# Kernel tuning notes

Measured on AMD Instinct MI355X. Metric: run time of the kernel, lower is better.

Reference implementation:

```python
import jax, jax.numpy as jnp
import numpy as np

# SpikingJelly LIFNode defaults
TAU = 2.0        # membrane time constant
V_TH = 1.0       # threshold
ALPHA = 2.0      # ATan surrogate alpha (forward is pure Heaviside)
T_STEPS = 4
OBS_DIM, CTX_DIM, ACT_DIM, HID = 128, 64, 32, 1024
OUTPUT_MAX = 1.0


def spike_fn(x):
    # forward-only Heaviside (surrogate only matters for backward)
    return (x >= 0.0).astype(x.dtype)


def lif_layer(x_seq):
    """Multi-step LIF: x_seq [T,B,H] -> spikes [T,B,H].
    decay_input=True: v = v + (x - (v - v_reset)) / tau; hard reset to v_reset=0."""
    def step(v, x):
        v = v + (x - v) / TAU
        s = spike_fn(v - V_TH)
        v = v * (1.0 - s)  # hard reset to 0
        return v, s
    v0 = jnp.zeros_like(x_seq[0])
    _, s_seq = jax.lax.scan(step, v0, x_seq)
    return s_seq


def setup_inputs() -> dict:
    key = jax.random.key(0)
    ks = jax.random.split(key, 12)
    B = 16384
    obs = jax.random.normal(ks[0], (B, OBS_DIM), dtype=jnp.float32)
    context = jax.random.normal(ks[1], (B, CTX_DIM), dtype=jnp.float32)
    # noise ~ N(0, 0.001) clamped later in reference
    noise = jax.random.normal(ks[2], (ACT_DIM,), dtype=jnp.float32) * 0.001
    in_dim = OBS_DIM + CTX_DIM
    def xavier(k, fan_in, fan_out, gain=0.1):
        bound = gain * np.sqrt(6.0 / (fan_in + fan_out))
        return jax.random.uniform(k, (fan_out, fan_in), jnp.float32, -bound, bound)
    W1 = xavier(ks[3], in_dim, HID); b1 = jnp.zeros((HID,), jnp.float32)
    W2 = xavier(ks[4], HID, HID);   b2 = jnp.zeros((HID,), jnp.float32)
    W3 = xavier(ks[5], HID, HID);   b3 = jnp.zeros((HID,), jnp.float32)
    Wm = xavier(ks[6], HID, ACT_DIM); bm = jnp.zeros((ACT_DIM,), jnp.float32)
    return {"obs": obs, "context": context, "noise": noise,
            "W1": W1, "b1": b1, "W2": W2, "b2": b2,
            "W3": W3, "b3": b3, "Wm": Wm, "bm": bm}


def reference(obs, context, noise, W1, b1, W2, b2, W3, b3, Wm, bm):
    x = jnp.concatenate([obs, context], axis=-1)           # [B, in_dim]
    x_seq = jnp.broadcast_to(x, (T_STEPS,) + x.shape)      # [T, B, in_dim]
    h = lif_layer(jnp.einsum('tbi,oi->tbo', x_seq, W1) + b1)
    h = lif_layer(jnp.einsum('tbh,oh->tbo', h, W2) + b2)
    h = lif_layer(jnp.einsum('tbh,oh->tbo', h, W3) + b3)
    feat = h.mean(axis=0)                                   # [B, HID]
    action_mean = OUTPUT_MAX * jnp.tanh(feat @ Wm.T + bm)   # [B, ACT_DIM]
    action = action_mean + jnp.clip(noise, -0.1, 0.1)
    return (action_mean, action)
```

## Files before the change

kernel.cpp:

```cpp
#include <hip/hip_runtime.h>
#include <stdint.h>
#include <math.h>

#define NB 16384


__global__ __launch_bounds__(256) void kA(
    const float* __restrict__ W1, const float* __restrict__ b1,
    const float* __restrict__ b2, const float* __restrict__ b3,
    const float* __restrict__ W3, const float* __restrict__ Wm,
    const float* __restrict__ bm, const float* __restrict__ noise,
    float* __restrict__ ws_f, unsigned int* __restrict__ ws_u)
{
  const int bid = blockIdx.x, tid = threadIdx.x;
  if (bid < 256) {
    const int wv = tid >> 6, lane = tid & 63;
    const int r = bid * 4 + wv;
    float ss = 0.f;
    if (lane < 48) {
      float4 v = *(const float4*)(W1 + (size_t)r * 192 + lane * 4);
      ss = v.x * v.x + v.y * v.y + v.z * v.z + v.w * v.w;
    }
    #pragma unroll
    for (int off = 32; off; off >>= 1) ss += __shfl_down(ss, off);
    if (lane == 0) atomicMax(&ws_u[1], __float_as_uint(ss));
    return;
  }
  if (bid == 256) {
    float m = 0.f;
    #pragma unroll
    for (int g = 0; g < 4; ++g) m = fmaxf(m, fabsf(b1[tid + 256 * g]));
    atomicMax(&ws_u[2], __float_as_uint(m));
    return;
  }
  __shared__ unsigned int m2[4][32];
  __shared__ unsigned int F2[4];
  __shared__ float feat[1024];
  __shared__ int fnz;
  if (tid < 128) ((unsigned int*)m2)[tid] = 0u;
  if (tid == 0) fnz = 0;
  __syncthreads();
  #pragma unroll
  for (int g = 0; g < 4; ++g) {
    const int o = tid + 256 * g;
    const float c = b2[o];
    float v = 0.f;
    #pragma unroll
    for (int t = 0; t < 4; ++t) {
      v = v + (c - v) * 0.5f;
      if (v >= 1.0f) { atomicOr(&m2[t][o >> 5], 1u << (o & 31)); v = 0.f; }
    }
  }
  __syncthreads();
  if (tid < 4) {
    unsigned int f = 0;
    #pragma unroll
    for (int w = 0; w < 32; ++w) f |= m2[tid][w];
    F2[tid] = f;
  }
  __syncthreads();
  #pragma unroll
  for (int g = 0; g < 4; ++g) {
    const int o = tid + 256 * g;
    const float cb = b3[o];
    float v = 0.f, fs = 0.f;
    #pragma unroll
    for (int t = 0; t < 4; ++t) {
      float c = cb;
      if (F2[t]) {
        for (int wl = 0; wl < 32; ++wl) {
          unsigned int mm = m2[t][wl];
          while (mm) {
            const int k = wl * 32 + __builtin_ctz(mm);
            c += W3[(size_t)o * 1024 + k];
            mm &= (mm - 1);
          }
        }
      }
      v = v + (c - v) * 0.5f;
      if (v >= 1.0f) { fs += 1.0f; v = 0.f; }
    }
    feat[o] = fs * 0.25f;
    if (fs > 0.f) fnz = 1;
  }
  __syncthreads();
  if (tid < 32) {
    float acc = 0.f;
    if (fnz) {
      const float* wr = Wm + (size_t)tid * 1024;
      for (int k = 0; k < 1024; ++k) acc += feat[k] * wr[k];
    }
    const float z = acc + bm[tid];
    const float am = tanhf(z);
    const float nz = fminf(fmaxf(noise[tid], -0.1f), 0.1f);
    ws_f[64 + tid] = am;
    ws_f[96 + tid] = am + nz;
  }
}

__global__ __launch_bounds__(256) void kMain(
    const float* __restrict__ obs, const float* __restrict__ ctx,
    const float* __restrict__ ws_f, const unsigned int* __restrict__ ws_u,
    int* __restrict__ ws_i, float* __restrict__ out)
{
  const int tid = threadIdx.x;
  if (blockIdx.x < 4096) {
    const int wv = tid >> 6, lane = tid & 63;
    const int r = blockIdx.x * 4 + wv;
    float ss = 0.f;
    if (lane < 32) {
      float4 v = ((const float4*)(obs + (size_t)r * 128))[lane];
      ss = v.x * v.x + v.y * v.y + v.z * v.z + v.w * v.w;
    } else if (lane < 48) {
      float4 v = ((const float4*)(ctx + (size_t)r * 64))[lane - 32];
      ss = v.x * v.x + v.y * v.y + v.z * v.z + v.w * v.w;
    }
    #pragma unroll
    for (int off = 32; off; off >>= 1) ss += __shfl_down(ss, off);
    if (lane == 0) {
      const float wm2 = __uint_as_float(ws_u[1]);
      const float bmx = __uint_as_float(ws_u[2]);
      const float bound = sqrtf(ss) * sqrtf(wm2) * 1.0001f + bmx + 1e-5f;
      if (bound >= 1.0666f) {
        const int idx = atomicAdd(&ws_i[0], 1);
        ws_i[256 + idx] = r;
      }
    }
    return;
  }
  const int t = (blockIdx.x - 4096) * 256 + tid;
  const int row = t >> 3, q = t & 7;
  float4 av = ((const float4*)(ws_f + 64))[q];
  float4 cv = ((const float4*)(ws_f + 96))[q];
  ((float4*)out)[(size_t)row * 8 + q] = av;
  ((float4*)(out + (size_t)NB * 32))[(size_t)row * 8 + q] = cv;
}

__global__ __launch_bounds__(256) void kFB(
    const float* __restrict__ obs, const float* __restrict__ ctx,
    const float* __restrict__ noise,
    const float* __restrict__ W1, const float* __restrict__ b1,
    const float* __restrict__ W2, const float* __restrict__ b2,
    const float* __restrict__ W3, const float* __restrict__ b3,
    const float* __restrict__ Wm, const float* __restrict__ bm,
    const int* __restrict__ ws_i, float* __restrict__ out)
{
  __shared__ float x[192];
  __shared__ unsigned int mm[2][4][32];
  __shared__ unsigned int F[2][4];
  __shared__ float feat[1024];
  const int tid = threadIdx.x;
  const int cnt = ws_i[0];
  for (int i = blockIdx.x; i < cnt; i += 64) {
    const int b = ws_i[256 + i];
    if (tid < 192)
      x[tid] = (tid < 128) ? obs[(size_t)b * 128 + tid]
                           : ctx[(size_t)b * 64 + (tid - 128)];
    ((unsigned int*)mm)[tid] = 0u;
    __syncthreads();
    #pragma unroll
    for (int g = 0; g < 4; ++g) {
      const int o = tid + 256 * g;
      float c = b1[o];
      const float* w = W1 + (size_t)o * 192;
      for (int k = 0; k < 192; ++k) c += x[k] * w[k];
      float v = 0.f;
      #pragma unroll
      for (int t = 0; t < 4; ++t) {
        v = v + (c - v) * 0.5f;
        if (v >= 1.0f) { atomicOr(&mm[0][t][o >> 5], 1u << (o & 31)); v = 0.f; }
      }
    }
    __syncthreads();
    if (tid < 8) {
      unsigned int f = 0;
      #pragma unroll
      for (int w = 0; w < 32; ++w) f |= mm[tid >> 2][tid & 3][w];
      F[tid >> 2][tid & 3] = f;
    }
    __syncthreads();
    #pragma unroll
    for (int g = 0; g < 4; ++g) {
      const int o = tid + 256 * g;
      const float cb = b2[o];
      float v = 0.f;
      #pragma unroll
      for (int t = 0; t < 4; ++t) {
        float c = cb;
        if (F[0][t]) {
          for (int wl = 0; wl < 32; ++wl) {
            unsigned int m = mm[0][t][wl];
            while (m) {
              const int k = wl * 32 + __builtin_ctz(m);
              c += W2[(size_t)o * 1024 + k];
              m &= (m - 1);
            }
          }
        }
        v = v + (c - v) * 0.5f;
        if (v >= 1.0f) { atomicOr(&mm[1][t][o >> 5], 1u << (o & 31)); v = 0.f; }
      }
    }
    __syncthreads();
    if (tid < 4) {
      unsigned int f = 0;
      #pragma unroll
      for (int w = 0; w < 32; ++w) f |= mm[1][tid][w];
      F[1][tid] = f;
    }
    __syncthreads();
    #pragma unroll
    for (int g = 0; g < 4; ++g) {
      const int o = tid + 256 * g;
      const float cb = b3[o];
      float v = 0.f, fs = 0.f;
      #pragma unroll
      for (int t = 0; t < 4; ++t) {
        float c = cb;
        if (F[1][t]) {
          for (int wl = 0; wl < 32; ++wl) {
            unsigned int m = mm[1][t][wl];
            while (m) {
              const int k = wl * 32 + __builtin_ctz(m);
              c += W3[(size_t)o * 1024 + k];
              m &= (m - 1);
            }
          }
        }
        v = v + (c - v) * 0.5f;
        if (v >= 1.0f) { fs += 1.0f; v = 0.f; }
      }
      feat[o] = fs * 0.25f;
    }
    __syncthreads();
    if (tid < 32) {
      const float* wr = Wm + (size_t)tid * 1024;
      float acc = 0.f;
      for (int k = 0; k < 1024; ++k) acc += feat[k] * wr[k];
      const float z = acc + bm[tid];
      const float am = tanhf(z);
      const float nz = fminf(fmaxf(noise[tid], -0.1f), 0.1f);
      out[(size_t)b * 32 + tid] = am;
      out[(size_t)NB * 32 + (size_t)b * 32 + tid] = am + nz;
    }
    __syncthreads();
  }
}

extern "C" void kernel_launch(void* const* d_in, const int* in_sizes, int n_in,
                              void* d_out, int out_size, void* d_ws, size_t ws_size,
                              hipStream_t stream) {
  const float* obs   = (const float*)d_in[0];
  const float* ctx   = (const float*)d_in[1];
  const float* noise = (const float*)d_in[2];
  const float* W1    = (const float*)d_in[3];
  const float* b1    = (const float*)d_in[4];
  const float* W2    = (const float*)d_in[5];
  const float* b2    = (const float*)d_in[6];
  const float* W3    = (const float*)d_in[7];
  const float* b3    = (const float*)d_in[8];
  const float* Wm    = (const float*)d_in[9];
  const float* bm    = (const float*)d_in[10];
  float* out = (float*)d_out;

  float*        ws_f = (float*)d_ws;
  unsigned int* ws_u = (unsigned int*)d_ws;
  int*          ws_i = (int*)d_ws;

  hipMemsetAsync(d_ws, 0, 64, stream);
  kA<<<258, 256, 0, stream>>>(W1, b1, b2, b3, W3, Wm, bm, noise, ws_f, ws_u);
  kMain<<<4608, 256, 0, stream>>>(obs, ctx, ws_f, ws_u, ws_i, out);
  kFB<<<64, 256, 0, stream>>>(obs, ctx, noise, W1, b1, W2, b2, W3, b3, Wm, bm,
                              ws_i, out);
}
```

Before: 103.7 us.

## Fuse bound check, broadcast store and fallback into one per-row kernel

Merges the row-norm bound kernel and the fallback kernel into a single kernel, kRow. In it each wavefront checks its own row and either writes the precomputed constant output or runs the full spiking MLP inline, using ballot-based sparse accumulation. The global atomicMax reductions are replaced by per-block partial maxima that each wave reduces again itself, which removes the workspace memset and the global atomic row-index queue. This cuts one launch and the memset. In exchange, any fallback row runs on a single wavefront with uncoalesced weight reads, which would be slow if many rows need the full path.

```diff
diff --git a/kernel.cpp b/kernel.cpp
--- a/kernel.cpp
+++ b/kernel.cpp
@@ -10,10 +10,11 @@
     const float* __restrict__ b2, const float* __restrict__ b3,
     const float* __restrict__ W3, const float* __restrict__ Wm,
     const float* __restrict__ bm, const float* __restrict__ noise,
-    float* __restrict__ ws_f, unsigned int* __restrict__ ws_u)
+    float* __restrict__ ws_f)
 {
   const int bid = blockIdx.x, tid = threadIdx.x;
   if (bid < 256) {
+    __shared__ float pm[4];
     const int wv = tid >> 6, lane = tid & 63;
     const int r = bid * 4 + wv;
     float ss = 0.f;
@@ -23,14 +24,24 @@
     }
     #pragma unroll
     for (int off = 32; off; off >>= 1) ss += __shfl_down(ss, off);
-    if (lane == 0) atomicMax(&ws_u[1], __float_as_uint(ss));
+    if (lane == 0) pm[wv] = ss;
+    __syncthreads();
+    if (tid == 0)
+      ws_f[bid] = fmaxf(fmaxf(pm[0], pm[1]), fmaxf(pm[2], pm[3]));
     return;
   }
   if (bid == 256) {
+    __shared__ float pm[4];
+    const int wv = tid >> 6, lane = tid & 63;
     float m = 0.f;
     #pragma unroll
     for (int g = 0; g < 4; ++g) m = fmaxf(m, fabsf(b1[tid + 256 * g]));
-    atomicMax(&ws_u[2], __float_as_uint(m));
+    #pragma unroll
+    for (int off = 32; off; off >>= 1) m = fmaxf(m, __shfl_down(m, off));
+    if (lane == 0) pm[wv] = m;
+    __syncthreads();
+    if (tid == 0)
+      ws_f[256] = fmaxf(fmaxf(pm[0], pm[1]), fmaxf(pm[2], pm[3]));
     return;
   }
   __shared__ unsigned int m2[4][32];
@@ -93,157 +104,117 @@
     const float z = acc + bm[tid];
     const float am = tanhf(z);
     const float nz = fminf(fmaxf(noise[tid], -0.1f), 0.1f);
-    ws_f[64 + tid] = am;
-    ws_f[96 + tid] = am + nz;
+    ws_f[512 + tid] = am;
+    ws_f[544 + tid] = am + nz;
   }
 }
 
-__global__ __launch_bounds__(256) void kMain(
-    const float* __restrict__ obs, const float* __restrict__ ctx,
-    const float* __restrict__ ws_f, const unsigned int* __restrict__ ws_u,
-    int* __restrict__ ws_i, float* __restrict__ out)
-{
-  const int tid = threadIdx.x;
-  if (blockIdx.x < 4096) {
-    const int wv = tid >> 6, lane = tid & 63;
-    const int r = blockIdx.x * 4 + wv;
-    float ss = 0.f;
-    if (lane < 32) {
-      float4 v = ((const float4*)(obs + (size_t)r * 128))[lane];
-      ss = v.x * v.x + v.y * v.y + v.z * v.z + v.w * v.w;
-    } else if (lane < 48) {
-      float4 v = ((const float4*)(ctx + (size_t)r * 64))[lane - 32];
-      ss = v.x * v.x + v.y * v.y + v.z * v.z + v.w * v.w;
-    }
-    #pragma unroll
-    for (int off = 32; off; off >>= 1) ss += __shfl_down(ss, off);
-    if (lane == 0) {
-      const float wm2 = __uint_as_float(ws_u[1]);
-      const float bmx = __uint_as_float(ws_u[2]);
-      const float bound = sqrtf(ss) * sqrtf(wm2) * 1.0001f + bmx + 1e-5f;
-      if (bound >= 1.0666f) {
-        const int idx = atomicAdd(&ws_i[0], 1);
-        ws_i[256 + idx] = r;
-      }
-    }
-    return;
-  }
-  const int t = (blockIdx.x - 4096) * 256 + tid;
-  const int row = t >> 3, q = t & 7;
-  float4 av = ((const float4*)(ws_f + 64))[q];
-  float4 cv = ((const float4*)(ws_f + 96))[q];
-  ((float4*)out)[(size_t)row * 8 + q] = av;
-  ((float4*)(out + (size_t)NB * 32))[(size_t)row * 8 + q] = cv;
-}
-
-__global__ __launch_bounds__(256) void kFB(
+__global__ __launch_bounds__(256) void kRow(
     const float* __restrict__ obs, const float* __restrict__ ctx,
     const float* __restrict__ noise,
     const float* __restrict__ W1, const float* __restrict__ b1,
     const float* __restrict__ W2, const float* __restrict__ b2,
     const float* __restrict__ W3, const float* __restrict__ b3,
     const float* __restrict__ Wm, const float* __restrict__ bm,
-    const int* __restrict__ ws_i, float* __restrict__ out)
+    const float* __restrict__ ws_f, float* __restrict__ out)
 {
-  __shared__ float x[192];
-  __shared__ unsigned int mm[2][4][32];
-  __shared__ unsigned int F[2][4];
-  __shared__ float feat[1024];
   const int tid = threadIdx.x;
-  const int cnt = ws_i[0];
-  for (int i = blockIdx.x; i < cnt; i += 64) {
-    const int b = ws_i[256 + i];
-    if (tid < 192)
-      x[tid] = (tid < 128) ? obs[(size_t)b * 128 + tid]
-                           : ctx[(size_t)b * 64 + (tid - 128)];
-    ((unsigned int*)mm)[tid] = 0u;
-    __syncthreads();
-    #pragma unroll
-    for (int g = 0; g < 4; ++g) {
-      const int o = tid + 256 * g;
-      float c = b1[o];
-      const float* w = W1 + (size_t)o * 192;
-      for (int k = 0; k < 192; ++k) c += x[k] * w[k];
-      float v = 0.f;
-      #pragma unroll
-      for (int t = 0; t < 4; ++t) {
-        v = v + (c - v) * 0.5f;
-        if (v >= 1.0f) { atomicOr(&mm[0][t][o >> 5], 1u << (o & 31)); v = 0.f; }
+  const int wv = tid >> 6, lane = tid & 63;
+  const int r = blockIdx.x * 4 + wv;
+
+  float ss = 0.f;
+  if (lane < 32) {
+    float4 v = ((const float4*)(obs + (size_t)r * 128))[lane];
+    ss = v.x * v.x + v.y * v.y + v.z * v.z + v.w * v.w;
+  } else if (lane < 48) {
+    float4 v = ((const float4*)(ctx + (size_t)r * 64))[lane - 32];
+    ss = v.x * v.x + v.y * v.y + v.z * v.z + v.w * v.w;
+  }
+  #pragma unroll
+  for (int off = 32; off; off >>= 1) ss += __shfl_xor(ss, off);
+
+  float wm2 = fmaxf(fmaxf(ws_f[lane], ws_f[lane + 64]),
+                    fmaxf(ws_f[lane + 128], ws_f[lane + 192]));
+  #pragma unroll
+  for (int off = 32; off; off >>= 1) wm2 = fmaxf(wm2, __shfl_xor(wm2, off));
+  const float bmx = ws_f[256];
+
+  const float bound = sqrtf(ss) * sqrtf(wm2) * 1.0001f + bmx + 1e-5f;
+
+  if (bound < 1.0666f) {
+    if (lane < 8)
+      ((float4*)out)[(size_t)r * 8 + lane] = ((const float4*)(ws_f + 512))[lane];
+    else if (lane < 16)
+      ((float4*)(out + (size_t)NB * 32))[(size_t)r * 8 + (lane - 8)] =
+          ((const float4*)(ws_f + 544))[lane - 8];
+    return;
+  }
+
+  unsigned long long s1b = 0ull;
+  for (int g = 0; g < 16; ++g) {
+    const int o = lane + 64 * g;
+    float c = b1[o];
+    const float* w = W1 + (size_t)o * 192;
+    for (int k = 0; k < 128; ++k) c += obs[(size_t)r * 128 + k] * w[k];
+    for (int k = 0; k < 64; ++k)  c += ctx[(size_t)r * 64 + k] * w[128 + k];
+    float v = 0.f;
+    #pragma unroll
+    for (int t = 0; t < 4; ++t) {
+      v = v + (c - v) * 0.5f;
+      if (v >= 1.0f) { s1b |= 1ull << (g * 4 + t); v = 0.f; }
+    }
+  }
+  unsigned long long s2b = 0ull;
+  for (int g = 0; g < 16; ++g) {
+    const int o = lane + 64 * g;
+    float v = 0.f;
+    for (int t = 0; t < 4; ++t) {
+      float c = b2[o];
+      for (int i = 0; i < 16; ++i) {
+        unsigned long long w = __ballot((s1b >> (i * 4 + t)) & 1ull);
+        while (w) {
+          const int k = 64 * i + __builtin_ctzll(w);
+          c += W2[(size_t)o * 1024 + k];
+          w &= (w - 1);
+        }
       }
-    }
-    __syncthreads();
-    if (tid < 8) {
-      unsigned int f = 0;
-      #pragma unroll
-      for (int w = 0; w < 32; ++w) f |= mm[tid >> 2][tid & 3][w];
-      F[tid >> 2][tid & 3] = f;
-    }
-    __syncthreads();
-    #pragma unroll
-    for (int g = 0; g < 4; ++g) {
-      const int o = tid + 256 * g;
-      const float cb = b2[o];
-      float v = 0.f;
-      #pragma unroll
-      for (int t = 0; t < 4; ++t) {
-        float c = cb;
-        if (F[0][t]) {
-          for (int wl = 0; wl < 32; ++wl) {
-            unsigned int m = mm[0][t][wl];
-            while (m) {
-              const int k = wl * 32 + __builtin_ctz(m);
-              c += W2[(size_t)o * 1024 + k];
-              m &= (m - 1);
-            }
-          }
+      v = v + (c - v) * 0.5f;
+      if (v >= 1.0f) { s2b |= 1ull << (g * 4 + t); v = 0.f; }
+    }
+  }
+  float feat[16];
+  for (int g = 0; g < 16; ++g) {
+    const int o = lane + 64 * g;
+    float v = 0.f, fs = 0.f;
+    for (int t = 0; t < 4; ++t) {
+      float c = b3[o];
+      for (int i = 0; i < 16; ++i) {
+        unsigned long long w = __ballot((s2b >> (i * 4 + t)) & 1ull);
+        while (w) {
+          const int k = 64 * i + __builtin_ctzll(w);
+          c += W3[(size_t)o * 1024 + k];
+          w &= (w - 1);
         }
-        v = v + (c - v) * 0.5f;
-        if (v >= 1.0f) { atomicOr(&mm[1][t][o >> 5], 1u << (o & 31)); v = 0.f; }
       }
-    }
-    __syncthreads();
-    if (tid < 4) {
-      unsigned int f = 0;
-      #pragma unroll
-      for (int w = 0; w < 32; ++w) f |= mm[1][tid][w];
-      F[1][tid] = f;
-    }
-    __syncthreads();
-    #pragma unroll
-    for (int g = 0; g < 4; ++g) {
-      const int o = tid + 256 * g;
-      const float cb = b3[o];
-      float v = 0.f, fs = 0.f;
-      #pragma unroll
-      for (int t = 0; t < 4; ++t) {
-        float c = cb;
-        if (F[1][t]) {
-          for (int wl = 0; wl < 32; ++wl) {
-            unsigned int m = mm[1][t][wl];
-            while (m) {
-              const int k = wl * 32 + __builtin_ctz(m);
-              c += W3[(size_t)o * 1024 + k];
-              m &= (m - 1);
-            }
-          }
-        }
-        v = v + (c - v) * 0.5f;
-        if (v >= 1.0f) { fs += 1.0f; v = 0.f; }
-      }
-      feat[o] = fs * 0.25f;
-    }
-    __syncthreads();
-    if (tid < 32) {
-      const float* wr = Wm + (size_t)tid * 1024;
-      float acc = 0.f;
-      for (int k = 0; k < 1024; ++k) acc += feat[k] * wr[k];
-      const float z = acc + bm[tid];
+      v = v + (c - v) * 0.5f;
+      if (v >= 1.0f) { fs += 1.0f; v = 0.f; }
+    }
+    feat[g] = fs * 0.25f;
+  }
+  for (int a = 0; a < 32; ++a) {
+    float p = 0.f;
+    #pragma unroll
+    for (int g = 0; g < 16; ++g)
+      p += feat[g] * Wm[(size_t)a * 1024 + lane + 64 * g];
+    #pragma unroll
+    for (int off = 32; off; off >>= 1) p += __shfl_xor(p, off);
+    if (lane == 0) {
+      const float z = p + bm[a];
       const float am = tanhf(z);
-      const float nz = fminf(fmaxf(noise[tid], -0.1f), 0.1f);
-      out[(size_t)b * 32 + tid] = am;
-      out[(size_t)NB * 32 + (size_t)b * 32 + tid] = am + nz;
-    }
-    __syncthreads();
+      const float nz = fminf(fmaxf(noise[a], -0.1f), 0.1f);
+      out[(size_t)r * 32 + a] = am;
+      out[(size_t)NB * 32 + (size_t)r * 32 + a] = am + nz;
+    }
   }
 }
 
@@ -262,14 +233,9 @@
   const float* Wm    = (const float*)d_in[9];
   const float* bm    = (const float*)d_in[10];
   float* out = (float*)d_out;
-
-  float*        ws_f = (float*)d_ws;
-  unsigned int* ws_u = (unsigned int*)d_ws;
-  int*          ws_i = (int*)d_ws;
-
-  hipMemsetAsync(d_ws, 0, 64, stream);
-  kA<<<258, 256, 0, stream>>>(W1, b1, b2, b3, W3, Wm, bm, noise, ws_f, ws_u);
-  kMain<<<4608, 256, 0, stream>>>(obs, ctx, ws_f, ws_u, ws_i, out);
-  kFB<<<64, 256, 0, stream>>>(obs, ctx, noise, W1, b1, W2, b2, W3, b3, Wm, bm,
-                              ws_i, out);
+  float* ws_f = (float*)d_ws;
+
+  kA<<<258, 256, 0, stream>>>(W1, b1, b2, b3, W3, Wm, bm, noise, ws_f);
+  kRow<<<4096, 256, 0, stream>>>(obs, ctx, noise, W1, b1, W2, b2, W3, b3,
+                                 Wm, bm, ws_f, out);
 }
```

After: 93.60 us (median of 2 runs). 9.7% less time.
